# Kernel optimization log

Measured on AMD Instinct MI355X. Metric: run time of the kernel, lower is better.

Reference implementation:

```python
import jax, jax.numpy as jnp
import numpy as np

N = 50000
E = 1_600_000
H = 4
IN_F = 256
OUT_F = 32
NEG_SLOPE = 0.2
EPS = 1e-8


def setup_inputs() -> dict:
    key = jax.random.key(0)
    k1, k2, k3, k4, k5 = jax.random.split(key, 5)
    x = jax.random.normal(k1, (N, IN_F), dtype=jnp.float32)
    edge_index = jax.random.randint(k2, (2, E), 0, N, dtype=jnp.int64)
    # Xavier-uniform-like scale for params
    wb = float(np.sqrt(6.0 / (IN_F + OUT_F)))
    ab = float(np.sqrt(6.0 / (OUT_F + 1)))
    W = jax.random.uniform(k3, (H, IN_F, OUT_F), dtype=jnp.float32, minval=-wb, maxval=wb)
    a_l = jax.random.uniform(k4, (H, OUT_F, 1), dtype=jnp.float32, minval=-ab, maxval=ab)
    a_r = jax.random.uniform(k5, (H, OUT_F, 1), dtype=jnp.float32, minval=-ab, maxval=ab)
    return {"x": x, "edge_index": edge_index, "W": W, "a_l": a_l, "a_r": a_r}


def reference(x, edge_index, W, a_l, a_r):
    n = x.shape[0]
    h = jnp.einsum('ni,hio->nho', x, W)                      # (N, H, O)
    attn_l = jnp.einsum('nho,hol->nh', h, a_l)               # (N, H)
    attn_r = jnp.einsum('nho,hol->nh', h, a_r)               # (N, H)
    src, dst = edge_index[0], edge_index[1]
    e = attn_l[src] + attn_r[dst]                            # (E, H)
    e = jnp.where(e >= 0, e, NEG_SLOPE * e)                  # leaky_relu
    # segment softmax over edges grouped by dst (global max, as in source)
    e_exp = jnp.exp(e - jnp.max(e))
    e_sum = jax.ops.segment_sum(e_exp, dst, num_segments=n)  # (N, H)
    alpha = e_exp / (e_sum[dst] + EPS)                       # (E, H)
    msg = h[src] * alpha[:, :, None]                         # (E, H, O)
    out = jax.ops.segment_sum(msg, dst, num_segments=n)      # (N, H, O)
    return out.reshape(n, H * OUT_F)                         # concat=True
```

## Files before the change

### kernel.cpp

```cpp
#include <hip/hip_runtime.h>

#define NN   50000
#define NE   1600000
#define FOUT 128
#define NCH  256
#define EPC  6250
#define NW   12500

typedef short s16x8 __attribute__((ext_vector_type(8)));
typedef float f32x4 __attribute__((ext_vector_type(4)));

#define OFF_M      0u
#define OFF_ROWPTR 16u
#define OFF_ROWCNT 50036u
#define OFF_C8     100036u
#define OFF_SEGB   3300036u
#define OFF_CSR    3400036u
#define OFF_H      4200036u
#define OFF_ATTL   7400036u
#define OFF_ATTR   7600036u
#define OFF_BP     7800036u

__device__ __forceinline__ unsigned short f2bf(float f) {
  unsigned u = __float_as_uint(f);
  u += 0x7FFFu + ((u >> 16) & 1u);
  return (unsigned short)(u >> 16);
}
__device__ __forceinline__ float bf2f(unsigned u) {
  return __uint_as_float(u << 16);
}
__device__ __forceinline__ unsigned enc_f32(float f) {
  unsigned u = __float_as_uint(f);
  return (u & 0x80000000u) ? ~u : (u | 0x80000000u);
}
__device__ __forceinline__ float dec_f32(unsigned u) {
  u = (u & 0x80000000u) ? (u & 0x7fffffffu) : ~u;
  return __uint_as_float(u);
}

__global__ __launch_bounds__(256) void k_repack(const float* __restrict__ W,
                                                unsigned* __restrict__ Bp) {
  const int f = blockIdx.x * 256 + threadIdx.x;
  const int s = f >> 9;
  const int c = (f >> 6) & 7;
  const int l = f & 63;
  const int hd = c >> 1;
  const int colw = (c & 1) * 16 + (l & 15);
  const int kb = s * 32 + (l >> 4) * 8;
  unsigned short t[8];
#pragma unroll
  for (int j = 0; j < 8; ++j)
    t[j] = f2bf(W[hd * 8192 + (kb + j) * 32 + colw]);
  uint4 o;
  o.x = (unsigned)t[0] | ((unsigned)t[1] << 16);
  o.y = (unsigned)t[2] | ((unsigned)t[3] << 16);
  o.z = (unsigned)t[4] | ((unsigned)t[5] << 16);
  o.w = (unsigned)t[6] | ((unsigned)t[7] << 16);
  reinterpret_cast<uint4*>(Bp)[f] = o;
}

__global__ __launch_bounds__(64) void k_gemm(const float* __restrict__ x,
                                             const uint4* __restrict__ Bp,
                                             const float* __restrict__ a_l,
                                             const float* __restrict__ a_r,
                                             unsigned short* __restrict__ h,
                                             float* __restrict__ attl,
                                             float* __restrict__ attr) {
  const int l = threadIdx.x;
  const int n0 = blockIdx.x * 32;
  const int lrow = l & 15, g = l >> 4;
  int r0 = n0 + lrow;      if (r0 >= NN) r0 = NN - 1;
  int r1 = n0 + 16 + lrow; if (r1 >= NN) r1 = NN - 1;
  const float* x0 = x + (size_t)r0 * 256 + g * 8;
  const float* x1 = x + (size_t)r1 * 256 + g * 8;
  f32x4 acc0[8], acc1[8];
#pragma unroll
  for (int c = 0; c < 8; ++c) {
    acc0[c] = (f32x4){0.f, 0.f, 0.f, 0.f};
    acc1[c] = (f32x4){0.f, 0.f, 0.f, 0.f};
  }
#pragma unroll
  for (int s = 0; s < 8; ++s) {
    union { s16x8 v; unsigned short u[8]; } a0, a1;
    const float4* p0 = reinterpret_cast<const float4*>(x0 + s * 32);
    const float4* p1 = reinterpret_cast<const float4*>(x1 + s * 32);
    float4 u00 = p0[0], u01 = p0[1];
    float4 u10 = p1[0], u11 = p1[1];
    a0.u[0] = f2bf(u00.x); a0.u[1] = f2bf(u00.y); a0.u[2] = f2bf(u00.z); a0.u[3] = f2bf(u00.w);
    a0.u[4] = f2bf(u01.x); a0.u[5] = f2bf(u01.y); a0.u[6] = f2bf(u01.z); a0.u[7] = f2bf(u01.w);
    a1.u[0] = f2bf(u10.x); a1.u[1] = f2bf(u10.y); a1.u[2] = f2bf(u10.z); a1.u[3] = f2bf(u10.w);
    a1.u[4] = f2bf(u11.x); a1.u[5] = f2bf(u11.y); a1.u[6] = f2bf(u11.z); a1.u[7] = f2bf(u11.w);
#pragma unroll
    for (int c = 0; c < 8; ++c) {
      union { uint4 q; s16x8 v; } b;
      b.q = Bp[(s * 8 + c) * 64 + l];
      acc0[c] = __builtin_amdgcn_mfma_f32_16x16x32_bf16(a0.v, b.v, acc0[c], 0, 0, 0);
      acc1[c] = __builtin_amdgcn_mfma_f32_16x16x32_bf16(a1.v, b.v, acc1[c], 0, 0, 0);
    }
  }
#pragma unroll
  for (int c = 0; c < 8; ++c) {
#pragma unroll
    for (int r = 0; r < 4; ++r) {
      const int na = n0 + g * 4 + r;
      if (na < NN) h[(size_t)na * FOUT + c * 16 + lrow] = f2bf(acc0[c][r]);
      const int nb = n0 + 16 + g * 4 + r;
      if (nb < NN) h[(size_t)nb * FOUT + c * 16 + lrow] = f2bf(acc1[c][r]);
    }
  }
  float al0[4], al1[4], ar0[4], ar1[4];
#pragma unroll
  for (int hd = 0; hd < 4; ++hd) {
    al0[hd] = a_l[hd * 32 + lrow];
    al1[hd] = a_l[hd * 32 + 16 + lrow];
    ar0[hd] = a_r[hd * 32 + lrow];
    ar1[hd] = a_r[hd * 32 + 16 + lrow];
  }
#pragma unroll
  for (int tile = 0; tile < 2; ++tile) {
    const int nbase = n0 + tile * 16 + g * 4;
#pragma unroll
    for (int r = 0; r < 4; ++r) {
#pragma unroll
      for (int hd = 0; hd < 4; ++hd) {
        const float c0 = tile ? acc1[2 * hd][r]     : acc0[2 * hd][r];
        const float c1 = tile ? acc1[2 * hd + 1][r] : acc0[2 * hd + 1][r];
        float pl = c0 * al0[hd] + c1 * al1[hd];
        float pr = c0 * ar0[hd] + c1 * ar1[hd];
#pragma unroll
        for (int m = 1; m < 16; m <<= 1) { pl += __shfl_xor(pl, m); pr += __shfl_xor(pr, m); }
        if (lrow == 0 && nbase + r < NN) {
          attl[(nbase + r) * 4 + hd] = pl;
          attr[(nbase + r) * 4 + hd] = pr;
        }
      }
    }
  }
}

__global__ __launch_bounds__(256) void k_histA(const int* __restrict__ ei,
                                               unsigned* __restrict__ c8) {
  __shared__ unsigned lh[NW];
  const int b = blockIdx.x, t = threadIdx.x;
  for (int w = t; w < NW; w += 256) lh[w] = 0u;
  __syncthreads();
  const int base = b * EPC;
  for (int k = 0; k < EPC; k += 256) {
    if (k + t < EPC) {
      const int d = ei[NE + base + k + t];
      atomicAdd(&lh[d >> 2], 1u << ((d & 3) * 8));
    }
  }
  __syncthreads();
  for (int w = t; w < NW; w += 256) c8[b * NW + w] = lh[w];
}

__global__ __launch_bounds__(256) void k_cscan1(unsigned* __restrict__ c8,
                                                unsigned* __restrict__ segb) {
  const int b = blockIdx.x;
  const int seg = b / 49;
  const int w = (b % 49) * 256 + threadIdx.x;
  if (w >= NW) return;
  unsigned R = 0;
  const int c0 = seg * 32;
#pragma unroll 4
  for (int c = 0; c < 32; ++c) {
    const unsigned tt = c8[(size_t)(c0 + c) * NW + w];
    c8[(size_t)(c0 + c) * NW + w] = R;
    R += tt;
  }
  segb[seg * NW + w] = R;
}

__global__ __launch_bounds__(256) void k_cscan2(unsigned* __restrict__ segb,
                                                unsigned* __restrict__ rowcnt) {
  const int w = blockIdx.x * 256 + threadIdx.x;
  if (w >= NW) return;
  unsigned R = 0;
#pragma unroll
  for (int s = 0; s < 8; ++s) {
    const unsigned tt = segb[s * NW + w];
    segb[s * NW + w] = R;
    R += tt;
  }
  uint4 rc;
  rc.x = R & 0xffu; rc.y = (R >> 8) & 0xffu; rc.z = (R >> 16) & 0xffu; rc.w = R >> 24;
  reinterpret_cast<uint4*>(rowcnt)[w] = rc;
}

__global__ __launch_bounds__(1024) void k_scan(const unsigned* __restrict__ counts,
                                               unsigned* __restrict__ row_ptr) {
  __shared__ unsigned sums[1024];
  const int t = threadIdx.x;
  const int CH = (NN + 1023) / 1024;
  const int lo = t * CH;
  const int hi = min(lo + CH, NN);
  unsigned s = 0;
  for (int i = lo; i < hi; ++i) s += counts[i];
  sums[t] = s;
  __syncthreads();
  for (int off = 1; off < 1024; off <<= 1) {
    unsigned v = (t >= off) ? sums[t - off] : 0u;
    __syncthreads();
    sums[t] += v;
    __syncthreads();
  }
  unsigned base = (t == 0) ? 0u : sums[t - 1];
  for (int i = lo; i < hi; ++i) { row_ptr[i] = base; base += counts[i]; }
  if (t == 0) row_ptr[NN] = sums[1023];
}

__global__ __launch_bounds__(256) void k_rank(const int* __restrict__ ei,
                                              const unsigned* __restrict__ c8,
                                              const unsigned* __restrict__ segb,
                                              const unsigned* __restrict__ row_ptr,
                                              const float* __restrict__ attl,
                                              const float* __restrict__ attr,
                                              unsigned short* __restrict__ csr,
                                              unsigned* __restrict__ Mslot) {
  __shared__ unsigned lh[NW];
  const int b = blockIdx.x, t = threadIdx.x;
  for (int w = t; w < NW; w += 256) lh[w] = 0u;
  __syncthreads();
  const int base = b * EPC;
  const unsigned* c8b = c8 + (size_t)b * NW;
  const unsigned* sgb = segb + (size_t)(b >> 5) * NW;
  const float4* AL = reinterpret_cast<const float4*>(attl);
  const float4* AR = reinterpret_cast<const float4*>(attr);
  float m = -3.4e38f;
  for (int k = 0; k < EPC; k += 256) {
    if (k + t < EPC) {
      const int e = base + k + t;
      const int s = ei[e];
      const int d = ei[NE + e];
      const int sh = (d & 3) * 8;
      const unsigned old = atomicAdd(&lh[d >> 2], 1u << sh);
      const unsigned lr = (old >> sh) & 0xffu;
      const unsigned cb = (c8b[d >> 2] >> sh) & 0xffu;
      const unsigned sb = (sgb[d >> 2] >> sh) & 0xffu;
      csr[row_ptr[d] + sb + cb + lr] = (unsigned short)s;
      const float4 a = AL[s];
      const float4 r = AR[d];
      float v0 = a.x + r.x, v1 = a.y + r.y, v2 = a.z + r.z, v3 = a.w + r.w;
      v0 = v0 >= 0.f ? v0 : 0.2f * v0;
      v1 = v1 >= 0.f ? v1 : 0.2f * v1;
      v2 = v2 >= 0.f ? v2 : 0.2f * v2;
      v3 = v3 >= 0.f ? v3 : 0.2f * v3;
      m = fmaxf(m, fmaxf(fmaxf(v0, v1), fmaxf(v2, v3)));
    }
  }
#pragma unroll
  for (int k = 32; k; k >>= 1) m = fmaxf(m, __shfl_xor(m, k));
  if ((t & 63) == 0) atomicMax(Mslot, enc_f32(m));
}

__global__ __launch_bounds__(256) void k_agg(const unsigned short* __restrict__ csr,
                                             const unsigned* __restrict__ row_ptr,
                                             const float* __restrict__ attl,
                                             const float* __restrict__ attr,
                                             const unsigned* __restrict__ hpk,
                                             const unsigned* __restrict__ Mslot,
                                             float* __restrict__ out) {
  const int t = threadIdx.x;
  const int n = blockIdx.x * 4 + (t >> 6);
  const int l = t & 63;
  const int hd = l >> 4;
  const float M = dec_f32(*Mslot);
  const float ar = attr[n * 4 + hd];
  const unsigned lo = row_ptr[n], hi = row_ptr[n + 1];
  float acc0 = 0.f, acc1 = 0.f, wsum = 0.f;
  unsigned i = lo;
  const unsigned nfull = (hi - lo) & ~7u;
  if (nfull) {
    unsigned sA[8]; float alA[8]; unsigned hvA[8];
#pragma unroll
    for (int j = 0; j < 8; ++j) sA[j] = csr[i + j];
#pragma unroll
    for (int j = 0; j < 8; ++j) {
      alA[j] = attl[(size_t)sA[j] * 4 + hd];
      hvA[j] = hpk[(size_t)sA[j] * 64 + l];
    }
    i += 8;
    while (i < lo + nfull) {
      unsigned sB[8]; float alB[8]; unsigned hvB[8];
#pragma unroll
      for (int j = 0; j < 8; ++j) sB[j] = csr[i + j];
#pragma unroll
      for (int j = 0; j < 8; ++j) {
        alB[j] = attl[(size_t)sB[j] * 4 + hd];
        hvB[j] = hpk[(size_t)sB[j] * 64 + l];
      }
#pragma unroll
      for (int j = 0; j < 8; ++j) {
        float v = alA[j] + ar; v = (v >= 0.f) ? v : 0.2f * v;
        const float w = __expf(v - M);
        acc0 = fmaf(w, bf2f(hvA[j] & 0xffffu), acc0);
        acc1 = fmaf(w, bf2f(hvA[j] >> 16), acc1);
        wsum += w;
      }
#pragma unroll
      for (int j = 0; j < 8; ++j) { alA[j] = alB[j]; hvA[j] = hvB[j]; }
      i += 8;
    }
#pragma unroll
    for (int j = 0; j < 8; ++j) {
      float v = alA[j] + ar; v = (v >= 0.f) ? v : 0.2f * v;
      const float w = __expf(v - M);
      acc0 = fmaf(w, bf2f(hvA[j] & 0xffffu), acc0);
      acc1 = fmaf(w, bf2f(hvA[j] >> 16), acc1);
      wsum += w;
    }
  }
  for (; i < hi; ++i) {
    const unsigned s = csr[i];
    const float al = attl[(size_t)s * 4 + hd];
    const unsigned hv = hpk[(size_t)s * 64 + l];
    float v = al + ar; v = (v >= 0.f) ? v : 0.2f * v;
    const float w = __expf(v - M);
    acc0 = fmaf(w, bf2f(hv & 0xffffu), acc0);
    acc1 = fmaf(w, bf2f(hv >> 16), acc1);
    wsum += w;
  }
  const float inv = 1.f / (wsum + 1e-8f);
  out[(size_t)n * FOUT + l * 2]     = acc0 * inv;
  out[(size_t)n * FOUT + l * 2 + 1] = acc1 * inv;
}

extern "C" void kernel_launch(void* const* d_in, const int* in_sizes, int n_in,
                              void* d_out, int out_size, void* d_ws, size_t ws_size,
                              hipStream_t stream) {
  const float* x   = (const float*)d_in[0];
  const int*   ei  = (const int*)d_in[1];
  const float* W   = (const float*)d_in[2];
  const float* a_l = (const float*)d_in[3];
  const float* a_r = (const float*)d_in[4];
  float* out = (float*)d_out;
  unsigned* ws = (unsigned*)d_ws;

  unsigned* Mslot   = ws + OFF_M;
  unsigned* row_ptr = ws + OFF_ROWPTR;
  unsigned* rowcnt  = ws + OFF_ROWCNT;
  unsigned* c8      = ws + OFF_C8;
  unsigned* segb    = ws + OFF_SEGB;
  unsigned short* csr = (unsigned short*)(ws + OFF_CSR);
  unsigned short* h = (unsigned short*)(ws + OFF_H);
  float*    attl    = (float*)(ws + OFF_ATTL);
  float*    attr    = (float*)(ws + OFF_ATTR);
  unsigned* Bp      = ws + OFF_BP;

  hipMemsetAsync(Mslot, 0, 16 * sizeof(unsigned), stream);

  k_repack<<<16, 256, 0, stream>>>(W, Bp);
  k_gemm  <<<(NN + 31) / 32, 64, 0, stream>>>(x, (const uint4*)Bp, a_l, a_r, h, attl, attr);
  k_histA <<<NCH, 256, 0, stream>>>(ei, c8);
  k_cscan1<<<392, 256, 0, stream>>>(c8, segb);
  k_cscan2<<<49, 256, 0, stream>>>(segb, rowcnt);
  k_scan  <<<1, 1024, 0, stream>>>(rowcnt, row_ptr);
  k_rank  <<<NCH, 256, 0, stream>>>(ei, c8, segb, row_ptr, attl, attr, csr, Mslot);
  k_agg   <<<NN / 4, 256, 0, stream>>>(csr, row_ptr, attl, attr,
                                       (const unsigned*)h, Mslot, out);
}
```

Measured before the change: 373.0 us.

## Fold attention vectors into GEMM, log2-domain softmax, wider agg lanes, bigger blocks

Precomputes W·a_l and W·a_r (scaled by log2e) as an extra bf16 MFMA B-tile, so the attention logits come out of the GEMM without shuffle reductions. The GEMM is restructured to one 16-row tile per wave with four waves per block and packed bf16 conversion via v_cvt_pk_bf16_f32. Aggregation now handles two nodes per wave, loads 4 features per lane, uses exp2 without subtracting the max, and rescales epsilon by 2^M instead. Histogram and rank kernels move to 1024-thread blocks, and the scan gets unroll hints. Skipping the max subtraction risks overflow or precision loss, and the bf16 logits lose accuracy relative to the fp32 dot product.

After: 353.0 us. 1.06x faster.

```diff
diff --git a/kernel.cpp b/kernel.cpp
--- a/kernel.cpp
+++ b/kernel.cpp
@@ -6,6 +6,7 @@
 #define NCH  256
 #define EPC  6250
 #define NW   12500
+#define LOG2E 1.4426950408889634f
 
 typedef short s16x8 __attribute__((ext_vector_type(8)));
 typedef float f32x4 __attribute__((ext_vector_type(4)));
@@ -20,14 +21,17 @@
 #define OFF_ATTL   7400036u
 #define OFF_ATTR   7600036u
 #define OFF_BP     7800036u
+#define OFF_BQ     7816420u
 
 __device__ __forceinline__ unsigned short f2bf(float f) {
   unsigned u = __float_as_uint(f);
   u += 0x7FFFu + ((u >> 16) & 1u);
   return (unsigned short)(u >> 16);
 }
-__device__ __forceinline__ float bf2f(unsigned u) {
-  return __uint_as_float(u << 16);
+__device__ __forceinline__ unsigned cvtpk(float lo, float hi) {
+  unsigned r;
+  asm("v_cvt_pk_bf16_f32 %0, %1, %2" : "=v"(r) : "v"(lo), "v"(hi));
+  return r;
 }
 __device__ __forceinline__ unsigned enc_f32(float f) {
   unsigned u = __float_as_uint(f);
@@ -59,100 +63,106 @@
   reinterpret_cast<uint4*>(Bp)[f] = o;
 }
 
-__global__ __launch_bounds__(64) void k_gemm(const float* __restrict__ x,
-                                             const uint4* __restrict__ Bp,
-                                             const float* __restrict__ a_l,
-                                             const float* __restrict__ a_r,
-                                             unsigned short* __restrict__ h,
-                                             float* __restrict__ attl,
-                                             float* __restrict__ attr) {
-  const int l = threadIdx.x;
-  const int n0 = blockIdx.x * 32;
+__global__ __launch_bounds__(256) void k_repack2(const float* __restrict__ W,
+                                                 const float* __restrict__ a_l,
+                                                 const float* __restrict__ a_r,
+                                                 unsigned* __restrict__ Bq) {
+  const int f = blockIdx.x * 256 + threadIdx.x;
+  const int s = f >> 6;
+  const int l = f & 63;
+  const int col = l & 15;
+  const int kb = s * 32 + (l >> 4) * 8;
+  unsigned short t[8];
+  if (col < 8) {
+    const int hd = col & 3;
+    const float* av = (col < 4 ? a_l : a_r) + hd * 32;
+#pragma unroll
+    for (int j = 0; j < 8; ++j) {
+      const float* wr = W + hd * 8192 + (size_t)(kb + j) * 32;
+      float dot = 0.f;
+#pragma unroll
+      for (int o = 0; o < 32; ++o) dot = fmaf(wr[o], av[o], dot);
+      t[j] = f2bf(dot * LOG2E);
+    }
+  } else {
+#pragma unroll
+    for (int j = 0; j < 8; ++j) t[j] = 0;
+  }
+  uint4 o;
+  o.x = (unsigned)t[0] | ((unsigned)t[1] << 16);
+  o.y = (unsigned)t[2] | ((unsigned)t[3] << 16);
+  o.z = (unsigned)t[4] | ((unsigned)t[5] << 16);
+  o.w = (unsigned)t[6] | ((unsigned)t[7] << 16);
+  reinterpret_cast<uint4*>(Bq)[f] = o;
+}
+
+__global__ __launch_bounds__(256) void k_gemm(const float* __restrict__ x,
+                                              const uint4* __restrict__ Bp,
+                                              const uint4* __restrict__ Bq,
+                                              unsigned short* __restrict__ h,
+                                              float* __restrict__ attl,
+                                              float* __restrict__ attr) {
+  const int t = threadIdx.x;
+  const int wid = t >> 6, l = t & 63;
+  const int n0 = (blockIdx.x * 4 + wid) * 16;
   const int lrow = l & 15, g = l >> 4;
-  int r0 = n0 + lrow;      if (r0 >= NN) r0 = NN - 1;
-  int r1 = n0 + 16 + lrow; if (r1 >= NN) r1 = NN - 1;
+  int r0 = n0 + lrow; if (r0 >= NN) r0 = NN - 1;
   const float* x0 = x + (size_t)r0 * 256 + g * 8;
-  const float* x1 = x + (size_t)r1 * 256 + g * 8;
-  f32x4 acc0[8], acc1[8];
-#pragma unroll
-  for (int c = 0; c < 8; ++c) {
-    acc0[c] = (f32x4){0.f, 0.f, 0.f, 0.f};
-    acc1[c] = (f32x4){0.f, 0.f, 0.f, 0.f};
-  }
+  f32x4 acc[8], acc9;
+#pragma unroll
+  for (int c = 0; c < 8; ++c) acc[c] = (f32x4){0.f, 0.f, 0.f, 0.f};
+  acc9 = (f32x4){0.f, 0.f, 0.f, 0.f};
 #pragma unroll
   for (int s = 0; s < 8; ++s) {
-    union { s16x8 v; unsigned short u[8]; } a0, a1;
-    const float4* p0 = reinterpret_cast<const float4*>(x0 + s * 32);
-    const float4* p1 = reinterpret_cast<const float4*>(x1 + s * 32);
-    float4 u00 = p0[0], u01 = p0[1];
-    float4 u10 = p1[0], u11 = p1[1];
-    a0.u[0] = f2bf(u00.x); a0.u[1] = f2bf(u00.y); a0.u[2] = f2bf(u00.z); a0.u[3] = f2bf(u00.w);
-    a0.u[4] = f2bf(u01.x); a0.u[5] = f2bf(u01.y); a0.u[6] = f2bf(u01.z); a0.u[7] = f2bf(u01.w);
-    a1.u[0] = f2bf(u10.x); a1.u[1] = f2bf(u10.y); a1.u[2] = f2bf(u10.z); a1.u[3] = f2bf(u10.w);
-    a1.u[4] = f2bf(u11.x); a1.u[5] = f2bf(u11.y); a1.u[6] = f2bf(u11.z); a1.u[7] = f2bf(u11.w);
+    const float4 u0 = *reinterpret_cast<const float4*>(x0 + s * 32);
+    const float4 u1 = *reinterpret_cast<const float4*>(x0 + s * 32 + 4);
+    union { s16x8 v; unsigned w[4]; } a;
+    a.w[0] = cvtpk(u0.x, u0.y);
+    a.w[1] = cvtpk(u0.z, u0.w);
+    a.w[2] = cvtpk(u1.x, u1.y);
+    a.w[3] = cvtpk(u1.z, u1.w);
 #pragma unroll
     for (int c = 0; c < 8; ++c) {
       union { uint4 q; s16x8 v; } b;
       b.q = Bp[(s * 8 + c) * 64 + l];
-      acc0[c] = __builtin_amdgcn_mfma_f32_16x16x32_bf16(a0.v, b.v, acc0[c], 0, 0, 0);
-      acc1[c] = __builtin_amdgcn_mfma_f32_16x16x32_bf16(a1.v, b.v, acc1[c], 0, 0, 0);
-    }
+      acc[c] = __builtin_amdgcn_mfma_f32_16x16x32_bf16(a.v, b.v, acc[c], 0, 0, 0);
+    }
+    union { uint4 q; s16x8 v; } b9;
+    b9.q = Bq[s * 64 + l];
+    acc9 = __builtin_amdgcn_mfma_f32_16x16x32_bf16(a.v, b9.v, acc9, 0, 0, 0);
   }
 #pragma unroll
   for (int c = 0; c < 8; ++c) {
 #pragma unroll
     for (int r = 0; r < 4; ++r) {
       const int na = n0 + g * 4 + r;
-      if (na < NN) h[(size_t)na * FOUT + c * 16 + lrow] = f2bf(acc0[c][r]);
-      const int nb = n0 + 16 + g * 4 + r;
-      if (nb < NN) h[(size_t)nb * FOUT + c * 16 + lrow] = f2bf(acc1[c][r]);
-    }
-  }
-  float al0[4], al1[4], ar0[4], ar1[4];
-#pragma unroll
-  for (int hd = 0; hd < 4; ++hd) {
-    al0[hd] = a_l[hd * 32 + lrow];
-    al1[hd] = a_l[hd * 32 + 16 + lrow];
-    ar0[hd] = a_r[hd * 32 + lrow];
-    ar1[hd] = a_r[hd * 32 + 16 + lrow];
-  }
-#pragma unroll
-  for (int tile = 0; tile < 2; ++tile) {
-    const int nbase = n0 + tile * 16 + g * 4;
+      if (na < NN) h[(size_t)na * FOUT + c * 16 + lrow] = f2bf(acc[c][r]);
+    }
+  }
+  if (lrow < 8) {
+    float* dst = (lrow < 4) ? attl : attr;
+    const int hd = lrow & 3;
 #pragma unroll
     for (int r = 0; r < 4; ++r) {
-#pragma unroll
-      for (int hd = 0; hd < 4; ++hd) {
-        const float c0 = tile ? acc1[2 * hd][r]     : acc0[2 * hd][r];
-        const float c1 = tile ? acc1[2 * hd + 1][r] : acc0[2 * hd + 1][r];
-        float pl = c0 * al0[hd] + c1 * al1[hd];
-        float pr = c0 * ar0[hd] + c1 * ar1[hd];
-#pragma unroll
-        for (int m = 1; m < 16; m <<= 1) { pl += __shfl_xor(pl, m); pr += __shfl_xor(pr, m); }
-        if (lrow == 0 && nbase + r < NN) {
-          attl[(nbase + r) * 4 + hd] = pl;
-          attr[(nbase + r) * 4 + hd] = pr;
-        }
-      }
-    }
-  }
-}
-
-__global__ __launch_bounds__(256) void k_histA(const int* __restrict__ ei,
-                                               unsigned* __restrict__ c8) {
+      const int na = n0 + g * 4 + r;
+      if (na < NN) dst[na * 4 + hd] = acc9[r];
+    }
+  }
+}
+
+__global__ __launch_bounds__(1024) void k_histA(const int* __restrict__ ei,
+                                                unsigned* __restrict__ c8) {
   __shared__ unsigned lh[NW];
   const int b = blockIdx.x, t = threadIdx.x;
-  for (int w = t; w < NW; w += 256) lh[w] = 0u;
+  for (int w = t; w < NW; w += 1024) lh[w] = 0u;
   __syncthreads();
   const int base = b * EPC;
-  for (int k = 0; k < EPC; k += 256) {
-    if (k + t < EPC) {
-      const int d = ei[NE + base + k + t];
-      atomicAdd(&lh[d >> 2], 1u << ((d & 3) * 8));
-    }
+  for (int k = t; k < EPC; k += 1024) {
+    const int d = ei[NE + base + k];
+    atomicAdd(&lh[d >> 2], 1u << ((d & 3) * 8));
   }
   __syncthreads();
-  for (int w = t; w < NW; w += 256) c8[b * NW + w] = lh[w];
+  for (int w = t; w < NW; w += 1024) c8[(size_t)b * NW + w] = lh[w];
 }
 
 __global__ __launch_bounds__(256) void k_cscan1(unsigned* __restrict__ c8,
@@ -196,6 +206,7 @@
   const int lo = t * CH;
   const int hi = min(lo + CH, NN);
   unsigned s = 0;
+#pragma unroll 7
   for (int i = lo; i < hi; ++i) s += counts[i];
   sums[t] = s;
   __syncthreads();
@@ -206,21 +217,22 @@
     __syncthreads();
   }
   unsigned base = (t == 0) ? 0u : sums[t - 1];
+#pragma unroll 7
   for (int i = lo; i < hi; ++i) { row_ptr[i] = base; base += counts[i]; }
   if (t == 0) row_ptr[NN] = sums[1023];
 }
 
-__global__ __launch_bounds__(256) void k_rank(const int* __restrict__ ei,
-                                              const unsigned* __restrict__ c8,
-                                              const unsigned* __restrict__ segb,
-                                              const unsigned* __restrict__ row_ptr,
-                                              const float* __restrict__ attl,
-                                              const float* __restrict__ attr,
-                                              unsigned short* __restrict__ csr,
-                                              unsigned* __restrict__ Mslot) {
+__global__ __launch_bounds__(1024) void k_rank(const int* __restrict__ ei,
+                                               const unsigned* __restrict__ c8,
+                                               const unsigned* __restrict__ segb,
+                                               const unsigned* __restrict__ row_ptr,
+                                               const float* __restrict__ attl,
+                                               const float* __restrict__ attr,
+                                               unsigned short* __restrict__ csr,
+                                               unsigned* __restrict__ Mslot) {
   __shared__ unsigned lh[NW];
   const int b = blockIdx.x, t = threadIdx.x;
-  for (int w = t; w < NW; w += 256) lh[w] = 0u;
+  for (int w = t; w < NW; w += 1024) lh[w] = 0u;
   __syncthreads();
   const int base = b * EPC;
   const unsigned* c8b = c8 + (size_t)b * NW;
@@ -228,26 +240,24 @@
   const float4* AL = reinterpret_cast<const float4*>(attl);
   const float4* AR = reinterpret_cast<const float4*>(attr);
   float m = -3.4e38f;
-  for (int k = 0; k < EPC; k += 256) {
-    if (k + t < EPC) {
-      const int e = base + k + t;
-      const int s = ei[e];
-      const int d = ei[NE + e];
-      const int sh = (d & 3) * 8;
-      const unsigned old = atomicAdd(&lh[d >> 2], 1u << sh);
-      const unsigned lr = (old >> sh) & 0xffu;
-      const unsigned cb = (c8b[d >> 2] >> sh) & 0xffu;
-      const unsigned sb = (sgb[d >> 2] >> sh) & 0xffu;
-      csr[row_ptr[d] + sb + cb + lr] = (unsigned short)s;
-      const float4 a = AL[s];
-      const float4 r = AR[d];
-      float v0 = a.x + r.x, v1 = a.y + r.y, v2 = a.z + r.z, v3 = a.w + r.w;
-      v0 = v0 >= 0.f ? v0 : 0.2f * v0;
-      v1 = v1 >= 0.f ? v1 : 0.2f * v1;
-      v2 = v2 >= 0.f ? v2 : 0.2f * v2;
-      v3 = v3 >= 0.f ? v3 : 0.2f * v3;
-      m = fmaxf(m, fmaxf(fmaxf(v0, v1), fmaxf(v2, v3)));
-    }
+  for (int k = t; k < EPC; k += 1024) {
+    const int e = base + k;
+    const int s = ei[e];
+    const int d = ei[NE + e];
+    const int sh = (d & 3) * 8;
+    const unsigned old = atomicAdd(&lh[d >> 2], 1u << sh);
+    const unsigned lr = (old >> sh) & 0xffu;
+    const unsigned cb = (c8b[d >> 2] >> sh) & 0xffu;
+    const unsigned sb = (sgb[d >> 2] >> sh) & 0xffu;
+    csr[row_ptr[d] + sb + cb + lr] = (unsigned short)s;
+    const float4 a = AL[s];
+    const float4 r = AR[d];
+    float v0 = a.x + r.x, v1 = a.y + r.y, v2 = a.z + r.z, v3 = a.w + r.w;
+    v0 = fmaxf(v0, 0.2f * v0);
+    v1 = fmaxf(v1, 0.2f * v1);
+    v2 = fmaxf(v2, 0.2f * v2);
+    v3 = fmaxf(v3, 0.2f * v3);
+    m = fmaxf(m, fmaxf(fmaxf(v0, v1), fmaxf(v2, v3)));
   }
 #pragma unroll
   for (int k = 32; k; k >>= 1) m = fmaxf(m, __shfl_xor(m, k));
@@ -262,68 +272,62 @@
                                              const unsigned* __restrict__ Mslot,
                                              float* __restrict__ out) {
   const int t = threadIdx.x;
-  const int n = blockIdx.x * 4 + (t >> 6);
-  const int l = t & 63;
-  const int hd = l >> 4;
-  const float M = dec_f32(*Mslot);
+  const int wid = t >> 6, l = t & 63;
+  const int q = l & 31;
+  const int n = blockIdx.x * 8 + wid * 2 + (l >> 5);
+  const int hd = q >> 3;
   const float ar = attr[n * 4 + hd];
-  const unsigned lo = row_ptr[n], hi = row_ptr[n + 1];
-  float acc0 = 0.f, acc1 = 0.f, wsum = 0.f;
-  unsigned i = lo;
-  const unsigned nfull = (hi - lo) & ~7u;
-  if (nfull) {
-    unsigned sA[8]; float alA[8]; unsigned hvA[8];
-#pragma unroll
-    for (int j = 0; j < 8; ++j) sA[j] = csr[i + j];
-#pragma unroll
-    for (int j = 0; j < 8; ++j) {
-      alA[j] = attl[(size_t)sA[j] * 4 + hd];
-      hvA[j] = hpk[(size_t)sA[j] * 64 + l];
-    }
-    i += 8;
-    while (i < lo + nfull) {
-      unsigned sB[8]; float alB[8]; unsigned hvB[8];
-#pragma unroll
-      for (int j = 0; j < 8; ++j) sB[j] = csr[i + j];
-#pragma unroll
-      for (int j = 0; j < 8; ++j) {
-        alB[j] = attl[(size_t)sB[j] * 4 + hd];
-        hvB[j] = hpk[(size_t)sB[j] * 64 + l];
-      }
-#pragma unroll
-      for (int j = 0; j < 8; ++j) {
-        float v = alA[j] + ar; v = (v >= 0.f) ? v : 0.2f * v;
-        const float w = __expf(v - M);
-        acc0 = fmaf(w, bf2f(hvA[j] & 0xffffu), acc0);
-        acc1 = fmaf(w, bf2f(hvA[j] >> 16), acc1);
-        wsum += w;
-      }
-#pragma unroll
-      for (int j = 0; j < 8; ++j) { alA[j] = alB[j]; hvA[j] = hvB[j]; }
-      i += 8;
-    }
-#pragma unroll
-    for (int j = 0; j < 8; ++j) {
-      float v = alA[j] + ar; v = (v >= 0.f) ? v : 0.2f * v;
-      const float w = __expf(v - M);
-      acc0 = fmaf(w, bf2f(hvA[j] & 0xffffu), acc0);
-      acc1 = fmaf(w, bf2f(hvA[j] >> 16), acc1);
-      wsum += w;
-    }
-  }
-  for (; i < hi; ++i) {
-    const unsigned s = csr[i];
-    const float al = attl[(size_t)s * 4 + hd];
-    const unsigned hv = hpk[(size_t)s * 64 + l];
-    float v = al + ar; v = (v >= 0.f) ? v : 0.2f * v;
-    const float w = __expf(v - M);
-    acc0 = fmaf(w, bf2f(hv & 0xffffu), acc0);
-    acc1 = fmaf(w, bf2f(hv >> 16), acc1);
-    wsum += w;
-  }
-  const float inv = 1.f / (wsum + 1e-8f);
-  out[(size_t)n * FOUT + l * 2]     = acc0 * inv;
-  out[(size_t)n * FOUT + l * 2 + 1] = acc1 * inv;
+  const float epsP = 1e-8f * __builtin_amdgcn_exp2f(dec_f32(*Mslot));
+  const unsigned lo = row_ptr[n];
+  const int deg = (int)(row_ptr[n + 1] - lo);
+  int mdeg = max(deg, __shfl_xor(deg, 32));
+  const int nb = (mdeg + 3) >> 2;
+  float acc0 = 0.f, acc1 = 0.f, acc2 = 0.f, acc3 = 0.f, wsum = 0.f;
+
+  float alA[4]; uint2 hvA[4];
+#define LOADB(BASE, alB, hvB)                                              \
+  {                                                                        \
+    _Pragma("unroll")                                                      \
+    for (int j = 0; j < 4; ++j) {                                          \
+      const int i = (BASE) + j;                                            \
+      unsigned idx = lo + (unsigned)((i < deg) ? i : 0);                   \
+      idx = (idx < NE) ? idx : (NE - 1);                                   \
+      const unsigned s = csr[idx];                                         \
+      const float a = attl[s * 4 + hd];                                    \
+      alB[j] = (i < deg) ? a : -1e30f;                                     \
+      hvB[j] = *reinterpret_cast<const uint2*>(&hpk[(size_t)s * 64 + q * 2]); \
+    }                                                                      \
+  }
+#define COMPUTE(alB, hvB)                                                  \
+  {                                                                        \
+    _Pragma("unroll")                                                      \
+    for (int j = 0; j < 4; ++j) {                                          \
+      const float v = alB[j] + ar;                                         \
+      const float w = __builtin_amdgcn_exp2f(fmaxf(v, 0.2f * v));          \
+      wsum += w;                                                           \
+      acc0 = fmaf(w, __uint_as_float(hvB[j].x << 16), acc0);               \
+      acc1 = fmaf(w, __uint_as_float(hvB[j].x & 0xffff0000u), acc1);       \
+      acc2 = fmaf(w, __uint_as_float(hvB[j].y << 16), acc2);               \
+      acc3 = fmaf(w, __uint_as_float(hvB[j].y & 0xffff0000u), acc3);       \
+    }                                                                      \
+  }
+  if (nb > 0) {
+    LOADB(0, alA, hvA);
+    for (int b = 1; b < nb; ++b) {
+      float alB[4]; uint2 hvB[4];
+      LOADB(b * 4, alB, hvB);
+      COMPUTE(alA, hvA);
+#pragma unroll
+      for (int j = 0; j < 4; ++j) { alA[j] = alB[j]; hvA[j] = hvB[j]; }
+    }
+    COMPUTE(alA, hvA);
+  }
+  const float inv = 1.f / (wsum + epsP);
+  float4 o;
+  o.x = acc0 * inv; o.y = acc1 * inv; o.z = acc2 * inv; o.w = acc3 * inv;
+  *reinterpret_cast<float4*>(&out[(size_t)n * FOUT + q * 4]) = o;
+#undef LOADB
+#undef COMPUTE
 }
 
 extern "C" void kernel_launch(void* const* d_in, const int* in_sizes, int n_in,
@@ -347,16 +351,19 @@
   float*    attl    = (float*)(ws + OFF_ATTL);
   float*    attr    = (float*)(ws + OFF_ATTR);
   unsigned* Bp      = ws + OFF_BP;
+  unsigned* Bq      = ws + OFF_BQ;
 
   hipMemsetAsync(Mslot, 0, 16 * sizeof(unsigned), stream);
 
-  k_repack<<<16, 256, 0, stream>>>(W, Bp);
-  k_gemm  <<<(NN + 31) / 32, 64, 0, stream>>>(x, (const uint4*)Bp, a_l, a_r, h, attl, attr);
-  k_histA <<<NCH, 256, 0, stream>>>(ei, c8);
-  k_cscan1<<<392, 256, 0, stream>>>(c8, segb);
-  k_cscan2<<<49, 256, 0, stream>>>(segb, rowcnt);
-  k_scan  <<<1, 1024, 0, stream>>>(rowcnt, row_ptr);
-  k_rank  <<<NCH, 256, 0, stream>>>(ei, c8, segb, row_ptr, attl, attr, csr, Mslot);
-  k_agg   <<<NN / 4, 256, 0, stream>>>(csr, row_ptr, attl, attr,
-                                       (const unsigned*)h, Mslot, out);
-}
+  k_repack <<<16, 256, 0, stream>>>(W, Bp);
+  k_repack2<<<2, 256, 0, stream>>>(W, a_l, a_r, Bq);
+  k_gemm   <<<(NN + 63) / 64, 256, 0, stream>>>(x, (const uint4*)Bp, (const uint4*)Bq,
+                                                h, attl, attr);
+  k_histA  <<<NCH, 1024, 0, stream>>>(ei, c8);
+  k_cscan1 <<<392, 256, 0, stream>>>(c8, segb);
+  k_cscan2 <<<49, 256, 0, stream>>>(segb, rowcnt);
+  k_scan   <<<1, 1024, 0, stream>>>(rowcnt, row_ptr);
+  k_rank   <<<NCH, 1024, 0, stream>>>(ei, c8, segb, row_ptr, attl, attr, csr, Mslot);
+  k_agg    <<<NN / 8, 256, 0, stream>>>(csr, row_ptr, attl, attr,
+                                        (const unsigned*)h, Mslot, out);
+}
```
